# Kernel tuning notes

Hardware: AMD Instinct MI355X
Metric: run time of the kernel (lower is better)

## Reference

```python
import jax, jax.numpy as jnp
import numpy as np

H = 16          # num_heads
WIN = 512       # window_size


def setup_inputs() -> dict:
    key = jax.random.key(0)
    ks = jax.random.split(key, 4)
    B, S, D = 1, 4096, 1024
    s = 1.0 / np.sqrt(D)
    x = jax.random.normal(ks[0], (B, S, D), jnp.float32)
    Wqkv = jax.random.normal(ks[1], (3 * D, D), jnp.float32) * s
    bqkv = jnp.zeros((3 * D,), jnp.float32)
    Wout = jax.random.normal(ks[2], (D, D), jnp.float32) * s
    bout = jnp.zeros((D,), jnp.float32)
    return {"x": x, "Wqkv": Wqkv, "bqkv": bqkv, "Wout": Wout, "bout": bout}


def reference(x, Wqkv, bqkv, Wout, bout):
    B, S, D = x.shape
    d = D // H
    pads = WIN // 2
    C = WIN                 # chunk of query tokens processed together
    N = S // C              # number of chunks
    L = C + WIN - 1         # key-block length covering all windows in a chunk

    qkv = (x @ Wqkv.T + bqkv).reshape(B, S, 3, H, d).transpose(2, 0, 3, 1, 4)
    q, k, v = qkv[0], qkv[1], qkv[2]          # [B,H,S,d]

    # zero-pad K/V exactly like F.pad(..., value=0.0) in the original
    kp = jnp.pad(k, ((0, 0), (0, 0), (pads, pads), (0, 0)))
    vp = jnp.pad(v, ((0, 0), (0, 0), (pads, pads), (0, 0)))

    # gather overlapping key/value blocks: chunk n covers padded idx [n*C, n*C+L)
    idx = jnp.arange(N)[:, None] * C + jnp.arange(L)[None, :]   # [N,L]
    kb = kp[:, :, idx, :]                      # [B,H,N,L,d]
    vb = vp[:, :, idx, :]
    qc = q.reshape(B, H, N, C, d)

    scores = jnp.einsum('bhncd,bhnld->bhncl', qc, kb) / np.sqrt(d).astype(np.float32)
    c = jnp.arange(C)[:, None]
    j = jnp.arange(L)[None, :]
    band = (j >= c) & (j < c + WIN)            # [C,L]; zero-pad keys stay IN (score 0), matching original
    scores = jnp.where(band, scores, -jnp.inf)
    attn = jax.nn.softmax(scores, axis=-1)

    o = jnp.einsum('bhncl,bhnld->bhncd', attn, vb).reshape(B, H, S, d)
    o = o.transpose(0, 2, 1, 3).reshape(B, S, D)
    return o @ Wout.T + bout
```

## Files before the change

kernel.cpp:

```cpp
#include <hip/hip_runtime.h>


typedef __bf16 bf16x8 __attribute__((ext_vector_type(8)));
typedef float f32x4 __attribute__((ext_vector_type(4)));
typedef unsigned short u16;
typedef unsigned int u32;

#define MFMA16(a, b, c) __builtin_amdgcn_mfma_f32_16x16x32_bf16(a, b, c, 0, 0, 0)

__device__ __forceinline__ u16 f2b(float f) {
  union { float f; u32 u; } x; x.f = f;
  u32 r = x.u + 0x7fffu + ((x.u >> 16) & 1u);
  return (u16)(r >> 16);
}

union U8x16 { int4 v; u16 u[8]; };

__device__ __forceinline__ void gll16(const u16* g, u16* l) {
  __builtin_amdgcn_global_load_lds(
      (const __attribute__((address_space(1))) u16*)g,
      (__attribute__((address_space(3))) u16*)l, 16, 0, 0);
}

__global__ void cvt_f32_bf16(const float* __restrict__ in, u16* __restrict__ out, int n8)
{
  const int i = blockIdx.x * blockDim.x + threadIdx.x;
  if (i >= n8) return;
  const float4 a = ((const float4*)in)[i * 2];
  const float4 b = ((const float4*)in)[i * 2 + 1];
  U8x16 t;
  t.u[0] = f2b(a.x); t.u[1] = f2b(a.y); t.u[2] = f2b(a.z); t.u[3] = f2b(a.w);
  t.u[4] = f2b(b.x); t.u[5] = f2b(b.y); t.u[6] = f2b(b.z); t.u[7] = f2b(b.w);
  ((int4*)out)[i] = t.v;
}

__global__ __launch_bounds__(256, 4) void gemm_qkv(
    const u16* __restrict__ A, const u16* __restrict__ B,
    const float* __restrict__ bias,
    u16* __restrict__ Qb, u16* __restrict__ Kp, u16* __restrict__ Vb)
{
  __shared__ u16 As[64 * 32];
  __shared__ u16 Bs[128 * 32];

  const int K = 1024;
  const int tid  = threadIdx.x;
  const int lane = tid & 63;
  const int wave = tid >> 6;
  const int quad = lane >> 4;
  const int c16  = lane & 15;
  const int wr   = wave >> 1;
  const int wc   = wave & 1;
  const long m0 = (long)blockIdx.y * 64;
  const long n0 = (long)blockIdx.x * 128;

  const int srA   = wave * 16 + (lane >> 2);
  const int srB   = wave * 32 + (lane >> 2);
  const int schunk = (lane & 3) ^ ((lane >> 3) & 3);
  const u16* gA0 = &A[(m0 + srA) * K + schunk * 8];
  const u16* gB0 = &B[(n0 + srB) * K + schunk * 8];
  const u16* gB1 = &B[(n0 + srB + 16) * K + schunk * 8];
  u16* const lA0 = &As[(wave * 16) * 32];
  u16* const lB0 = &Bs[(wave * 32) * 32];
  u16* const lB1 = &Bs[(wave * 32 + 16) * 32];

  const int cs = (quad ^ ((c16 >> 1) & 3)) * 8;
  const u16* pa[2]; const u16* pb[4];
#pragma unroll
  for (int i = 0; i < 2; ++i) pa[i] = &As[(wr * 32 + i * 16 + c16) * 32 + cs];
#pragma unroll
  for (int j = 0; j < 4; ++j) pb[j] = &Bs[(wc * 64 + j * 16 + c16) * 32 + cs];

  f32x4 acc[2][4];
#pragma unroll
  for (int i = 0; i < 2; ++i)
#pragma unroll
    for (int j = 0; j < 4; ++j)
      acc[i][j] = f32x4{0.f, 0.f, 0.f, 0.f};

  for (int k0 = 0; k0 < K; k0 += 32) {
    __syncthreads();
    gll16(gA0, lA0);
    gll16(gB0, lB0); gll16(gB1, lB1);
    gA0 += 32; gB0 += 32; gB1 += 32;
    __syncthreads();

    bf16x8 af[2], bfr[4];
#pragma unroll
    for (int i = 0; i < 2; ++i) af[i]  = *(const bf16x8*)pa[i];
#pragma unroll
    for (int j = 0; j < 4; ++j) bfr[j] = *(const bf16x8*)pb[j];
#pragma unroll
    for (int i = 0; i < 2; ++i)
#pragma unroll
      for (int j = 0; j < 4; ++j)
        acc[i][j] = MFMA16(af[i], bfr[j], acc[i][j]);
  }

  const int region = (int)(n0 >> 10);
#pragma unroll
  for (int i = 0; i < 2; ++i) {
    const long row0 = m0 + wr * 32 + i * 16 + quad * 4;
#pragma unroll
    for (int j = 0; j < 4; ++j) {
      const long col = n0 + wc * 64 + j * 16 + c16;
      const float bv = bias[col];
#pragma unroll
      for (int r = 0; r < 4; ++r) {
        const u16 v = f2b(acc[i][j][r] + bv);
        const long row = row0 + r;
        if (region == 0) {
          Qb[row * 1024 + col] = v;
        } else if (region == 1) {
          const int n1 = (int)(col - 1024);
          const int h = n1 >> 6, d = n1 & 63;
          Kp[((long)h * 4608 + row + 256) * 64 + d] = v;
        } else {
          Vb[row * 1024 + (col - 2048)] = v;
        }
      }
    }
  }
}

__global__ __launch_bounds__(256, 4) void gemm_out(
    const u16* __restrict__ A, const u16* __restrict__ B,
    const float* __restrict__ bias, float* __restrict__ C)
{
  __shared__ u16 As[64 * 32];
  __shared__ u16 Bs[64 * 32];

  const int K = 1024, N = 1024;
  const int tid  = threadIdx.x;
  const int lane = tid & 63;
  const int wave = tid >> 6;
  const int quad = lane >> 4;
  const int c16  = lane & 15;
  const int wr   = wave >> 1;
  const int wc   = wave & 1;
  const long m0 = (long)blockIdx.y * 64;
  const long n0 = (long)blockIdx.x * 64;

  const int srow   = wave * 16 + (lane >> 2);
  const int schunk = (lane & 3) ^ ((lane >> 3) & 3);
  const u16* gA0 = &A[(m0 + srow) * K + schunk * 8];
  const u16* gB0 = &B[(n0 + srow) * K + schunk * 8];
  u16* const lA0 = &As[(wave * 16) * 32];
  u16* const lB0 = &Bs[(wave * 16) * 32];

  const int cs = (quad ^ ((c16 >> 1) & 3)) * 8;
  const u16* pa[2]; const u16* pb[2];
#pragma unroll
  for (int i = 0; i < 2; ++i) {
    pa[i] = &As[(wr * 32 + i * 16 + c16) * 32 + cs];
    pb[i] = &Bs[(wc * 32 + i * 16 + c16) * 32 + cs];
  }

  f32x4 acc[2][2];
#pragma unroll
  for (int i = 0; i < 2; ++i)
#pragma unroll
    for (int j = 0; j < 2; ++j)
      acc[i][j] = f32x4{0.f, 0.f, 0.f, 0.f};

  for (int k0 = 0; k0 < K; k0 += 32) {
    __syncthreads();
    gll16(gA0, lA0);
    gll16(gB0, lB0);
    gA0 += 32; gB0 += 32;
    __syncthreads();

    bf16x8 af[2], bfr[2];
#pragma unroll
    for (int i = 0; i < 2; ++i) af[i]  = *(const bf16x8*)pa[i];
#pragma unroll
    for (int j = 0; j < 2; ++j) bfr[j] = *(const bf16x8*)pb[j];
#pragma unroll
    for (int i = 0; i < 2; ++i)
#pragma unroll
      for (int j = 0; j < 2; ++j)
        acc[i][j] = MFMA16(af[i], bfr[j], acc[i][j]);
  }

#pragma unroll
  for (int i = 0; i < 2; ++i) {
    const long row0 = m0 + wr * 32 + i * 16 + quad * 4;
#pragma unroll
    for (int j = 0; j < 2; ++j) {
      const long col = n0 + wc * 32 + j * 16 + c16;
      const float bv = bias[col];
#pragma unroll
      for (int r = 0; r < 4; ++r)
        C[(row0 + r) * N + col] = acc[i][j][r] + bv;
    }
  }
}

__global__ __launch_bounds__(256, 2) void repack_v(
    const u16* __restrict__ Vb, u16* __restrict__ Kp, u16* __restrict__ VTp)
{
  __shared__ u16 lds[64 * 64];
  const int tile = blockIdx.x;
  const int h    = blockIdx.y;
  const int tid  = threadIdx.x;
  const int kt   = tile * 64 - 256;
  const long vtb = (long)h * 64 * 4608;

  if (kt < 0 || kt >= 4096) {
    const int4 z = {0, 0, 0, 0};
    for (int idx = tid; idx < 512; idx += 256) {
      const int r = idx >> 3, c = idx & 7;
      *(int4*)(&Kp[((long)h * 4608 + tile * 64 + r) * 64 + c * 8]) = z;
      *(int4*)(&VTp[vtb + (long)r * 4608 + tile * 64 + c * 8])     = z;
    }
    return;
  }

  for (int idx = tid; idx < 512; idx += 256) {
    const int r = idx >> 3, c = idx & 7;
    U8x16 t; t.v = *(const int4*)(&Vb[(long)(kt + r) * 1024 + h * 64 + c * 8]);
#pragma unroll
    for (int j = 0; j < 8; ++j) {
      const int d = c * 8 + j;
      lds[d * 64 + (((r >> 3) ^ ((c + j) & 7)) * 8) + (r & 7)] = t.u[j];
    }
  }
  __syncthreads();
  for (int idx = tid; idx < 512; idx += 256) {
    const int d = idx >> 3, c2 = idx & 7;
    const int sl = (c2 ^ ((d + (d >> 3)) & 7)) * 8;
    const int4 v = *(const int4*)(&lds[d * 64 + sl]);
    *(int4*)(&VTp[vtb + (long)d * 4608 + 256 + kt + c2 * 8]) = v;
  }
}

__global__ __launch_bounds__(512, 4) void swa_fused(
    const u16* __restrict__ Qb, const u16* __restrict__ Kp,
    const u16* __restrict__ VTp, u16* __restrict__ o)
{
  __shared__ u16 Ks[64 * 64];
  __shared__ u16 Vs[64 * 64];
  __shared__ u16 Ps[8 * 16 * 64];

  const int tid  = threadIdx.x;
  const int lane = tid & 63;
  const int w    = tid >> 6;
  const int quad = lane >> 4;
  const int c16  = lane & 15;
  const int h    = blockIdx.y;
  const int qb0  = blockIdx.x * 128;

  const long qrow = qb0 + w * 16 + c16;
  const bf16x8 aq0 = *(const bf16x8*)(&Qb[qrow * 1024 + h * 64 + quad * 8]);
  const bf16x8 aq1 = *(const bf16x8*)(&Qb[qrow * 1024 + h * 64 + 32 + quad * 8]);

  const int srow   = w * 8 + (lane >> 3);
  const int gchunk = (lane & 7) ^ (lane >> 3);
  const u16* gK = &Kp[((long)h * 4608 + qb0 + srow) * 64 + gchunk * 8];
  const u16* gV = &VTp[((long)h * 64 + srow) * 4608 + qb0 + gchunk * 8];
  u16* const lK = &Ks[(w * 8) * 64];
  u16* const lV = &Vs[(w * 8) * 64];

  const int rsw = c16 & 7;
  const u16* pK[4][2]; const u16* pV[4][2];
#pragma unroll
  for (int t16 = 0; t16 < 4; ++t16) {
    pK[t16][0] = &Ks[(t16 * 16 + c16) * 64 + (quad ^ rsw) * 8];
    pK[t16][1] = &Ks[(t16 * 16 + c16) * 64 + ((4 + quad) ^ rsw) * 8];
    pV[t16][0] = &Vs[(t16 * 16 + c16) * 64 + (quad ^ rsw) * 8];
    pV[t16][1] = &Vs[(t16 * 16 + c16) * 64 + ((4 + quad) ^ rsw) * 8];
  }
  u16* const Pw  = &Ps[w * 1024];
  const u16* pP0 = &Ps[w * 1024 + c16 * 64 + (quad ^ rsw) * 8];
  const u16* pP1 = &Ps[w * 1024 + c16 * 64 + ((4 + quad) ^ rsw) * 8];

  const int t_lo = w >> 2;
  const int t_hi = 8 + (w >> 2);
  const int dbase = c16 - 16 * w - quad * 4;

  f32x4 acc[4];
#pragma unroll
  for (int dt = 0; dt < 4; ++dt) acc[dt] = f32x4{0.f, 0.f, 0.f, 0.f};
  float rsum[4] = {0.f, 0.f, 0.f, 0.f};

  for (int t = 0; t < 10; ++t) {
    __syncthreads();
    gll16(gK, lK); gll16(gV, lV);
    gK += 64 * 64; gV += 64;
    __syncthreads();
    if (t < t_lo || t > t_hi) continue;

#pragma unroll
    for (int tcol = 0; tcol < 4; ++tcol) {
      const bf16x8 bk0 = *(const bf16x8*)pK[tcol][0];
      const bf16x8 bk1 = *(const bf16x8*)pK[tcol][1];
      f32x4 s = f32x4{0.f, 0.f, 0.f, 0.f};
      s = MFMA16(aq0, bk0, s);
      s = MFMA16(aq1, bk1, s);
#pragma unroll
      for (int r = 0; r < 4; ++r) {
        const int delta = dbase + t * 64 + tcol * 16 - r;
        const float p = ((u32)delta < 512u) ? __expf(s[r] * 0.125f) : 0.f;
        rsum[r] += p;
        const int q  = quad * 4 + r;
        const int kc = tcol * 16 + c16;
        Pw[q * 64 + (((kc >> 3) ^ (q & 7)) * 8) + (kc & 7)] = f2b(p);
      }
    }

    const bf16x8 ap0 = *(const bf16x8*)pP0;
    const bf16x8 ap1 = *(const bf16x8*)pP1;
#pragma unroll
    for (int dt = 0; dt < 4; ++dt) {
      const bf16x8 bv0 = *(const bf16x8*)pV[dt][0];
      const bf16x8 bv1 = *(const bf16x8*)pV[dt][1];
      acc[dt] = MFMA16(ap0, bv0, acc[dt]);
      acc[dt] = MFMA16(ap1, bv1, acc[dt]);
    }
  }

#pragma unroll
  for (int off = 1; off < 16; off <<= 1)
#pragma unroll
    for (int r = 0; r < 4; ++r)
      rsum[r] += __shfl_xor(rsum[r], off, 64);

  const int qp = qb0 + w * 16 + quad * 4;
#pragma unroll
  for (int r = 0; r < 4; ++r) {
    const float inv = 1.f / rsum[r];
#pragma unroll
    for (int dt = 0; dt < 4; ++dt)
      o[(long)(qp + r) * 1024 + h * 64 + dt * 16 + c16] = f2b(acc[dt][r] * inv);
  }
}

extern "C" void kernel_launch(void* const* d_in, const int* in_sizes, int n_in,
                              void* d_out, int out_size, void* d_ws, size_t ws_size,
                              hipStream_t stream)
{
  const float* x    = (const float*)d_in[0];
  const float* Wqkv = (const float*)d_in[1];
  const float* bqkv = (const float*)d_in[2];
  const float* Wout = (const float*)d_in[3];
  const float* bout = (const float*)d_in[4];
  float* out = (float*)d_out;

  u16* xb    = (u16*)d_ws;
  u16* wqkvb = xb    + (size_t)4096 * 1024;
  u16* woutb = wqkvb + (size_t)3072 * 1024;
  u16* Qb    = woutb + (size_t)1024 * 1024;
  u16* Kp    = Qb    + (size_t)4096 * 1024;
  u16* VTp   = Kp    + (size_t)16 * 4608 * 64;
  u16* Vb    = VTp   + (size_t)16 * 4608 * 64;
  u16* o     = Vb;

  cvt_f32_bf16<<<4096 * 1024 / 8 / 256, 256, 0, stream>>>(x, xb, 4096 * 1024 / 8);
  cvt_f32_bf16<<<3072 * 1024 / 8 / 256, 256, 0, stream>>>(Wqkv, wqkvb, 3072 * 1024 / 8);
  cvt_f32_bf16<<<1024 * 1024 / 8 / 256, 256, 0, stream>>>(Wout, woutb, 1024 * 1024 / 8);

  gemm_qkv<<<dim3(3072 / 128, 4096 / 64), 256, 0, stream>>>(
      xb, wqkvb, bqkv, Qb, Kp, Vb);
  repack_v<<<dim3(72, 16), 256, 0, stream>>>(Vb, Kp, VTp);
  swa_fused<<<dim3(4096 / 128, 16), 512, 0, stream>>>(Qb, Kp, VTp, o);
  gemm_out<<<dim3(1024 / 64, 4096 / 64), 256, 0, stream>>>(o, woutb, bout, out);
}
```

Measured before the change: 181.4 us.

## Double GEMM K-tile to 64 and shrink attention blocks to 64 queries

Both GEMMs now stage K-tiles of 64 instead of 32, with an 8-chunk XOR swizzle. This halves the number of barrier-synchronised load/compute iterations and gives twice as many MFMAs per sync, at the cost of more LDS per block. The attention kernel moves to 256-thread blocks covering 64 queries, with each wave loading two rows. Its loop shrinks from 10 to 9 key tiles with no per-wave skipping, so waves no longer idle on out-of-window tiles, and the grid doubles.

```diff
diff --git a/kernel.cpp b/kernel.cpp
--- a/kernel.cpp
+++ b/kernel.cpp
@@ -39,8 +39,8 @@
     const float* __restrict__ bias,
     u16* __restrict__ Qb, u16* __restrict__ Kp, u16* __restrict__ Vb)
 {
-  __shared__ u16 As[64 * 32];
-  __shared__ u16 Bs[128 * 32];
+  __shared__ u16 As[64 * 64];
+  __shared__ u16 Bs[128 * 64];
 
   const int K = 1024;
   const int tid  = threadIdx.x;
@@ -53,22 +53,33 @@
   const long m0 = (long)blockIdx.y * 64;
   const long n0 = (long)blockIdx.x * 128;
 
-  const int srA   = wave * 16 + (lane >> 2);
-  const int srB   = wave * 32 + (lane >> 2);
-  const int schunk = (lane & 3) ^ ((lane >> 3) & 3);
-  const u16* gA0 = &A[(m0 + srA) * K + schunk * 8];
-  const u16* gB0 = &B[(n0 + srB) * K + schunk * 8];
-  const u16* gB1 = &B[(n0 + srB + 16) * K + schunk * 8];
-  u16* const lA0 = &As[(wave * 16) * 32];
-  u16* const lB0 = &Bs[(wave * 32) * 32];
-  u16* const lB1 = &Bs[(wave * 32 + 16) * 32];
-
-  const int cs = (quad ^ ((c16 >> 1) & 3)) * 8;
-  const u16* pa[2]; const u16* pb[4];
-#pragma unroll
-  for (int i = 0; i < 2; ++i) pa[i] = &As[(wr * 32 + i * 16 + c16) * 32 + cs];
-#pragma unroll
-  for (int j = 0; j < 4; ++j) pb[j] = &Bs[(wc * 64 + j * 16 + c16) * 32 + cs];
+  const int rowo   = lane >> 3;
+  const int schunk = (lane & 7) ^ rowo;
+  const u16* gA0 = &A[(m0 + wave * 16 + rowo) * K + schunk * 8];
+  const u16* gA1 = gA0 + 8 * K;
+  const u16* gB0 = &B[(n0 + wave * 32 + rowo) * K + schunk * 8];
+  const u16* gB1 = gB0 + 8 * K;
+  const u16* gB2 = gB0 + 16 * K;
+  const u16* gB3 = gB0 + 24 * K;
+  u16* const lA0 = &As[(wave * 16) * 64];
+  u16* const lA1 = lA0 + 8 * 64;
+  u16* const lB0 = &Bs[(wave * 32) * 64];
+  u16* const lB1 = lB0 + 8 * 64;
+  u16* const lB2 = lB0 + 16 * 64;
+  u16* const lB3 = lB0 + 24 * 64;
+
+  const int rsw = c16 & 7;
+  const u16* pa[2][2]; const u16* pb[4][2];
+#pragma unroll
+  for (int i = 0; i < 2; ++i) {
+    pa[i][0] = &As[(wr * 32 + i * 16 + c16) * 64 + (quad ^ rsw) * 8];
+    pa[i][1] = &As[(wr * 32 + i * 16 + c16) * 64 + ((4 + quad) ^ rsw) * 8];
+  }
+#pragma unroll
+  for (int j = 0; j < 4; ++j) {
+    pb[j][0] = &Bs[(wc * 64 + j * 16 + c16) * 64 + (quad ^ rsw) * 8];
+    pb[j][1] = &Bs[(wc * 64 + j * 16 + c16) * 64 + ((4 + quad) ^ rsw) * 8];
+  }
 
   f32x4 acc[2][4];
 #pragma unroll
@@ -77,23 +88,26 @@
     for (int j = 0; j < 4; ++j)
       acc[i][j] = f32x4{0.f, 0.f, 0.f, 0.f};
 
-  for (int k0 = 0; k0 < K; k0 += 32) {
-    __syncthreads();
-    gll16(gA0, lA0);
-    gll16(gB0, lB0); gll16(gB1, lB1);
-    gA0 += 32; gB0 += 32; gB1 += 32;
-    __syncthreads();
-
-    bf16x8 af[2], bfr[4];
-#pragma unroll
-    for (int i = 0; i < 2; ++i) af[i]  = *(const bf16x8*)pa[i];
-#pragma unroll
-    for (int j = 0; j < 4; ++j) bfr[j] = *(const bf16x8*)pb[j];
-#pragma unroll
-    for (int i = 0; i < 2; ++i)
-#pragma unroll
-      for (int j = 0; j < 4; ++j)
-        acc[i][j] = MFMA16(af[i], bfr[j], acc[i][j]);
+  for (int k0 = 0; k0 < K; k0 += 64) {
+    __syncthreads();
+    gll16(gA0, lA0); gll16(gA1, lA1);
+    gll16(gB0, lB0); gll16(gB1, lB1); gll16(gB2, lB2); gll16(gB3, lB3);
+    gA0 += 64; gA1 += 64; gB0 += 64; gB1 += 64; gB2 += 64; gB3 += 64;
+    __syncthreads();
+
+#pragma unroll
+    for (int h = 0; h < 2; ++h) {
+      bf16x8 af[2], bfr[4];
+#pragma unroll
+      for (int i = 0; i < 2; ++i) af[i]  = *(const bf16x8*)pa[i][h];
+#pragma unroll
+      for (int j = 0; j < 4; ++j) bfr[j] = *(const bf16x8*)pb[j][h];
+#pragma unroll
+      for (int i = 0; i < 2; ++i)
+#pragma unroll
+        for (int j = 0; j < 4; ++j)
+          acc[i][j] = MFMA16(af[i], bfr[j], acc[i][j]);
+    }
   }
 
   const int region = (int)(n0 >> 10);
@@ -126,8 +140,8 @@
     const u16* __restrict__ A, const u16* __restrict__ B,
     const float* __restrict__ bias, float* __restrict__ C)
 {
-  __shared__ u16 As[64 * 32];
-  __shared__ u16 Bs[64 * 32];
+  __shared__ u16 As[64 * 64];
+  __shared__ u16 Bs[64 * 64];
 
   const int K = 1024, N = 1024;
   const int tid  = threadIdx.x;
@@ -140,19 +154,25 @@
   const long m0 = (long)blockIdx.y * 64;
   const long n0 = (long)blockIdx.x * 64;
 
-  const int srow   = wave * 16 + (lane >> 2);
-  const int schunk = (lane & 3) ^ ((lane >> 3) & 3);
-  const u16* gA0 = &A[(m0 + srow) * K + schunk * 8];
-  const u16* gB0 = &B[(n0 + srow) * K + schunk * 8];
-  u16* const lA0 = &As[(wave * 16) * 32];
-  u16* const lB0 = &Bs[(wave * 16) * 32];
-
-  const int cs = (quad ^ ((c16 >> 1) & 3)) * 8;
-  const u16* pa[2]; const u16* pb[2];
+  const int rowo   = lane >> 3;
+  const int schunk = (lane & 7) ^ rowo;
+  const u16* gA0 = &A[(m0 + wave * 16 + rowo) * K + schunk * 8];
+  const u16* gA1 = gA0 + 8 * K;
+  const u16* gB0 = &B[(n0 + wave * 16 + rowo) * K + schunk * 8];
+  const u16* gB1 = gB0 + 8 * K;
+  u16* const lA0 = &As[(wave * 16) * 64];
+  u16* const lA1 = lA0 + 8 * 64;
+  u16* const lB0 = &Bs[(wave * 16) * 64];
+  u16* const lB1 = lB0 + 8 * 64;
+
+  const int rsw = c16 & 7;
+  const u16* pa[2][2]; const u16* pb[2][2];
 #pragma unroll
   for (int i = 0; i < 2; ++i) {
-    pa[i] = &As[(wr * 32 + i * 16 + c16) * 32 + cs];
-    pb[i] = &Bs[(wc * 32 + i * 16 + c16) * 32 + cs];
+    pa[i][0] = &As[(wr * 32 + i * 16 + c16) * 64 + (quad ^ rsw) * 8];
+    pa[i][1] = &As[(wr * 32 + i * 16 + c16) * 64 + ((4 + quad) ^ rsw) * 8];
+    pb[i][0] = &Bs[(wc * 32 + i * 16 + c16) * 64 + (quad ^ rsw) * 8];
+    pb[i][1] = &Bs[(wc * 32 + i * 16 + c16) * 64 + ((4 + quad) ^ rsw) * 8];
   }
 
   f32x4 acc[2][2];
@@ -162,23 +182,26 @@
     for (int j = 0; j < 2; ++j)
       acc[i][j] = f32x4{0.f, 0.f, 0.f, 0.f};
 
-  for (int k0 = 0; k0 < K; k0 += 32) {
-    __syncthreads();
-    gll16(gA0, lA0);
-    gll16(gB0, lB0);
-    gA0 += 32; gB0 += 32;
-    __syncthreads();
-
-    bf16x8 af[2], bfr[2];
-#pragma unroll
-    for (int i = 0; i < 2; ++i) af[i]  = *(const bf16x8*)pa[i];
-#pragma unroll
-    for (int j = 0; j < 2; ++j) bfr[j] = *(const bf16x8*)pb[j];
-#pragma unroll
-    for (int i = 0; i < 2; ++i)
-#pragma unroll
-      for (int j = 0; j < 2; ++j)
-        acc[i][j] = MFMA16(af[i], bfr[j], acc[i][j]);
+  for (int k0 = 0; k0 < K; k0 += 64) {
+    __syncthreads();
+    gll16(gA0, lA0); gll16(gA1, lA1);
+    gll16(gB0, lB0); gll16(gB1, lB1);
+    gA0 += 64; gA1 += 64; gB0 += 64; gB1 += 64;
+    __syncthreads();
+
+#pragma unroll
+    for (int h = 0; h < 2; ++h) {
+      bf16x8 af[2], bfr[2];
+#pragma unroll
+      for (int i = 0; i < 2; ++i) af[i]  = *(const bf16x8*)pa[i][h];
+#pragma unroll
+      for (int j = 0; j < 2; ++j) bfr[j] = *(const bf16x8*)pb[j][h];
+#pragma unroll
+      for (int i = 0; i < 2; ++i)
+#pragma unroll
+        for (int j = 0; j < 2; ++j)
+          acc[i][j] = MFMA16(af[i], bfr[j], acc[i][j]);
+    }
   }
 
 #pragma unroll
@@ -233,13 +256,13 @@
   }
 }
 
-__global__ __launch_bounds__(512, 4) void swa_fused(
+__global__ __launch_bounds__(256, 4) void swa_fused(
     const u16* __restrict__ Qb, const u16* __restrict__ Kp,
     const u16* __restrict__ VTp, u16* __restrict__ o)
 {
   __shared__ u16 Ks[64 * 64];
   __shared__ u16 Vs[64 * 64];
-  __shared__ u16 Ps[8 * 16 * 64];
+  __shared__ u16 Ps[4 * 16 * 64];
 
   const int tid  = threadIdx.x;
   const int lane = tid & 63;
@@ -247,18 +270,22 @@
   const int quad = lane >> 4;
   const int c16  = lane & 15;
   const int h    = blockIdx.y;
-  const int qb0  = blockIdx.x * 128;
+  const int qb0  = blockIdx.x * 64;
 
   const long qrow = qb0 + w * 16 + c16;
   const bf16x8 aq0 = *(const bf16x8*)(&Qb[qrow * 1024 + h * 64 + quad * 8]);
   const bf16x8 aq1 = *(const bf16x8*)(&Qb[qrow * 1024 + h * 64 + 32 + quad * 8]);
 
-  const int srow   = w * 8 + (lane >> 3);
-  const int gchunk = (lane & 7) ^ (lane >> 3);
-  const u16* gK = &Kp[((long)h * 4608 + qb0 + srow) * 64 + gchunk * 8];
-  const u16* gV = &VTp[((long)h * 64 + srow) * 4608 + qb0 + gchunk * 8];
-  u16* const lK = &Ks[(w * 8) * 64];
-  u16* const lV = &Vs[(w * 8) * 64];
+  const int rowo   = lane >> 3;
+  const int gchunk = (lane & 7) ^ rowo;
+  const u16* gK0 = &Kp[((long)h * 4608 + qb0 + w * 16 + rowo) * 64 + gchunk * 8];
+  const u16* gK1 = gK0 + 8 * 64;
+  const u16* gV0 = &VTp[((long)h * 64 + w * 16 + rowo) * 4608 + qb0 + gchunk * 8];
+  const u16* gV1 = gV0 + 8 * 4608;
+  u16* const lK0 = &Ks[(w * 16) * 64];
+  u16* const lK1 = lK0 + 8 * 64;
+  u16* const lV0 = &Vs[(w * 16) * 64];
+  u16* const lV1 = lV0 + 8 * 64;
 
   const int rsw = c16 & 7;
   const u16* pK[4][2]; const u16* pV[4][2];
@@ -273,8 +300,6 @@
   const u16* pP0 = &Ps[w * 1024 + c16 * 64 + (quad ^ rsw) * 8];
   const u16* pP1 = &Ps[w * 1024 + c16 * 64 + ((4 + quad) ^ rsw) * 8];
 
-  const int t_lo = w >> 2;
-  const int t_hi = 8 + (w >> 2);
   const int dbase = c16 - 16 * w - quad * 4;
 
   f32x4 acc[4];
@@ -282,12 +307,12 @@
   for (int dt = 0; dt < 4; ++dt) acc[dt] = f32x4{0.f, 0.f, 0.f, 0.f};
   float rsum[4] = {0.f, 0.f, 0.f, 0.f};
 
-  for (int t = 0; t < 10; ++t) {
-    __syncthreads();
-    gll16(gK, lK); gll16(gV, lV);
-    gK += 64 * 64; gV += 64;
-    __syncthreads();
-    if (t < t_lo || t > t_hi) continue;
+  for (int t = 0; t < 9; ++t) {
+    __syncthreads();
+    gll16(gK0, lK0); gll16(gK1, lK1);
+    gll16(gV0, lV0); gll16(gV1, lV1);
+    gK0 += 64 * 64; gK1 += 64 * 64; gV0 += 64; gV1 += 64;
+    __syncthreads();
 
 #pragma unroll
     for (int tcol = 0; tcol < 4; ++tcol) {
@@ -361,6 +386,6 @@
   gemm_qkv<<<dim3(3072 / 128, 4096 / 64), 256, 0, stream>>>(
       xb, wqkvb, bqkv, Qb, Kp, Vb);
   repack_v<<<dim3(72, 16), 256, 0, stream>>>(Vb, Kp, VTp);
-  swa_fused<<<dim3(4096 / 128, 16), 512, 0, stream>>>(Qb, Kp, VTp, o);
+  swa_fused<<<dim3(4096 / 64, 16), 256, 0, stream>>>(Qb, Kp, VTp, o);
   gemm_out<<<dim3(1024 / 64, 4096 / 64), 256, 0, stream>>>(o, woutb, bout, out);
 }
```

Result: faster. 167.0 us (-7.9%).
